# Kernel optimization log

Measured on AMD Instinct MI355X. Metric: run time of the kernel, lower is better.

## Reference

```python
import jax, jax.numpy as jnp
import numpy as np

B, I, H, N, E, SEQ = 16, 128, 32, 2048, 32768, 100


def setup_inputs() -> dict:
    key = jax.random.key(0)
    ks = jax.random.split(key, 8)
    s = lambda fan: 1.0 / np.sqrt(fan)
    return {
        "x": jax.random.normal(ks[0], (B, I), jnp.float32),
        "src": jax.random.randint(ks[1], (E,), 0, N, jnp.int32),
        "dst": jax.random.randint(ks[2], (E,), 0, N, jnp.int32),
        "Wr": jax.random.normal(ks[3], (I, H), jnp.float32) * s(I),
        "br": jnp.zeros((H,), jnp.float32),
        "Wz": jax.random.normal(ks[4], (I, H), jnp.float32) * s(I),
        "bz": jnp.zeros((H,), jnp.float32),
        "Wh": jax.random.normal(ks[5], (I, H), jnp.float32) * s(I),
        "bh": jnp.zeros((H,), jnp.float32),
        "Wg": jax.random.normal(ks[6], (H, H), jnp.float32) * s(H),
        "bg": jnp.zeros((H,), jnp.float32),
    }


def reference(x, src, dst, Wr, br, Wz, bz, Wh, bh, Wg, bg):
    # DGL GraphConv norm='both': edge weight 1/sqrt(deg_out[src]*deg_in[dst])
    ones = jnp.ones((E,), jnp.float32)
    deg_out = jnp.clip(jax.ops.segment_sum(ones, src, num_segments=N), 1.0)
    deg_in = jnp.clip(jax.ops.segment_sum(ones, dst, num_segments=N), 1.0)
    enorm = jax.lax.rsqrt(deg_out[src] * deg_in[dst])  # [E]

    # Input gates are constant over time (x is a single context vector)
    xr = (x @ Wr + br)[:, None, :]  # [B,1,H]
    xz = (x @ Wz + bz)[:, None, :]
    xh = (x @ Wh + bh)[:, None, :]

    def step(h, _):
        # message passing: gather src, normalize, scatter-add to dst
        m = h[:, src, :] * enorm[None, :, None]            # [B,E,H]
        agg = jnp.zeros_like(h).at[:, dst, :].add(m)       # [B,N,H]
        h_conv = agg @ Wg + bg                             # [B,N,H]
        r = jax.nn.sigmoid(xr + h_conv)
        z = jax.nn.sigmoid(xz + h_conv)
        h_tilde = jnp.tanh(xh + r * h_conv)
        h_new = (1.0 - z) * h + z * h_tilde
        return h_new, h_new

    h0 = jnp.zeros((B, N, H), jnp.float32)
    _, outs = jax.lax.scan(step, h0, None, length=SEQ)     # [SEQ,B,N,H]
    return jnp.transpose(outs, (1, 0, 2, 3)).reshape(B, -1)
```

## Files before the change

kernel.cpp:

```cpp
#include <hip/hip_runtime.h>
#include <math.h>

#define BATCH 16
#define IN 128
#define HD 32
#define NN 2048
#define NE 32768
#define SEQ 100
#define TPB 512
#define NBLK 512
#define GSZ 32
#define NGRP (NBLK / GSZ)
#define NXCD 8
#define MAXJ 64
#define ECAP 1536


__global__ void count_deg(const int* __restrict__ src, const int* __restrict__ dst,
                          int* deg_out, int* deg_in) {
    int e = blockIdx.x * blockDim.x + threadIdx.x;
    if (e < NE) {
        atomicAdd(&deg_out[src[e]], 1);
        atomicAdd(&deg_in[dst[e]], 1);
    }
}

__global__ void scan_rowptr(const int* __restrict__ deg_in, int* __restrict__ row_ptr) {
    __shared__ int partial[256];
    int t = threadIdx.x;
    int base = t * 8;
    int vals[8];
    int s = 0;
    for (int j = 0; j < 8; j++) { vals[j] = deg_in[base + j]; s += vals[j]; }
    partial[t] = s;
    __syncthreads();
    if (t == 0) {
        int acc = 0;
        for (int i = 0; i < 256; i++) { int v = partial[i]; partial[i] = acc; acc += v; }
        row_ptr[NN] = acc;
    }
    __syncthreads();
    int acc = partial[t];
    for (int j = 0; j < 8; j++) { row_ptr[base + j] = acc; acc += vals[j]; }
}

__global__ void scatter_edges(const int* __restrict__ src, const int* __restrict__ dst,
                              const int* __restrict__ deg_out, const int* __restrict__ deg_in,
                              const int* __restrict__ row_ptr, int* __restrict__ cursor,
                              int* __restrict__ col_idx, float* __restrict__ wgt) {
    int e = blockIdx.x * blockDim.x + threadIdx.x;
    if (e < NE) {
        int s = src[e], d = dst[e];
        int pos = row_ptr[d] + atomicAdd(&cursor[d], 1);
        col_idx[pos] = s * HD;
        float doo = (float)max(deg_out[s], 1);
        float dii = (float)max(deg_in[d], 1);
        wgt[pos] = rsqrtf(doo * dii);
    }
}

__global__ void xgates(const float* __restrict__ x,
                       const float* __restrict__ Wr, const float* __restrict__ br,
                       const float* __restrict__ Wz, const float* __restrict__ bz,
                       const float* __restrict__ Wh, const float* __restrict__ bh,
                       float* __restrict__ xr, float* __restrict__ xz, float* __restrict__ xh) {
    int t = blockIdx.x * blockDim.x + threadIdx.x;
    if (t < BATCH * HD) {
        int b = t / HD, hh = t % HD;
        float ar = br[hh], az = bz[hh], ah = bh[hh];
        const float* xb = x + b * IN;
        for (int i = 0; i < IN; i++) {
            float xv = xb[i];
            ar += xv * Wr[i * HD + hh];
            az += xv * Wz[i * HD + hh];
            ah += xv * Wh[i * HD + hh];
        }
        xr[t] = ar; xz[t] = az; xh[t] = ah;
    }
}


__device__ __forceinline__ void global_barrier(unsigned* __restrict__ lvl1,
                                               unsigned* __restrict__ root,
                                               unsigned step) {
    __syncthreads();
    if (threadIdx.x == 0) {
        const int gid = blockIdx.x / GSZ;
        __builtin_amdgcn_fence(__ATOMIC_RELEASE, "agent");
        __hip_atomic_fetch_add(&lvl1[gid * 32], 1u, __ATOMIC_RELAXED,
                               __HIP_MEMORY_SCOPE_AGENT);
        if ((blockIdx.x % GSZ) == 0) {
            while (__hip_atomic_load(&lvl1[gid * 32], __ATOMIC_RELAXED,
                                     __HIP_MEMORY_SCOPE_AGENT) < GSZ * step)
                __builtin_amdgcn_s_sleep(2);
            __hip_atomic_fetch_add(root, 1u, __ATOMIC_RELAXED,
                                   __HIP_MEMORY_SCOPE_AGENT);
        }
        while (__hip_atomic_load(root, __ATOMIC_RELAXED,
                                 __HIP_MEMORY_SCOPE_AGENT) < NGRP * step)
            __builtin_amdgcn_s_sleep(2);
        __builtin_amdgcn_fence(__ATOMIC_ACQUIRE, "agent");
    }
    __syncthreads();
}

__device__ __forceinline__ void xcd_barrier(unsigned* __restrict__ xcnt,
                                            unsigned* __restrict__ xgo,
                                            int xid, int slot, int cnt, unsigned s) {
    __syncthreads();
    if (threadIdx.x == 0) {
        __hip_atomic_fetch_add(&xcnt[xid * 32], 1u, __ATOMIC_RELAXED,
                               __HIP_MEMORY_SCOPE_AGENT);
        if (slot == 0) {
            while (__hip_atomic_load(&xcnt[xid * 32], __ATOMIC_RELAXED,
                                     __HIP_MEMORY_SCOPE_AGENT) < (unsigned)cnt * s)
                __builtin_amdgcn_s_sleep(1);
            __hip_atomic_store(&xgo[xid * 32], s, __ATOMIC_RELAXED,
                               __HIP_MEMORY_SCOPE_AGENT);
        } else {
            while (__hip_atomic_load(&xgo[xid * 32], __ATOMIC_RELAXED,
                                     __HIP_MEMORY_SCOPE_AGENT) < s)
                __builtin_amdgcn_s_sleep(1);
        }
    }
    __syncthreads();
    asm volatile("buffer_inv sc0\n\ts_waitcnt vmcnt(0)" ::: "memory");
}


__device__ __forceinline__ float fast_sigmoid(float x) {
    return __builtin_amdgcn_rcpf(1.f + __expf(-x));
}

__global__ void __launch_bounds__(TPB) gru_persistent(
    float* __restrict__ hA, float* __restrict__ hB,
    const int* __restrict__ row_ptr, const int* __restrict__ col_idx,
    const float* __restrict__ wgt,
    const float* __restrict__ Wg, const float* __restrict__ bg,
    const float* __restrict__ xr, const float* __restrict__ xz,
    const float* __restrict__ xh,
    float* __restrict__ out,
    unsigned* __restrict__ glvl1, unsigned* __restrict__ groot,
    unsigned* __restrict__ xreg, unsigned* __restrict__ xcnt,
    unsigned* __restrict__ xgo)
{
    __shared__ float aggL[TPB];
    __shared__ int jn[MAXJ], jrs[MAXJ], jraw[MAXJ], jplen[MAXJ], jofs[MAXJ];
    __shared__ __align__(16) int2 eLDS[ECAP];
    __shared__ int shr_slot, shr_cnt, shr_mode, shr_use;

    const int tid = threadIdx.x;
    const int lane = tid & 63;
    const int wid = tid >> 6;
    const int half = lane >> 5;
    const int l = lane & 31;

    int xraw;
    asm volatile("s_getreg_b32 %0, hwreg(HW_REG_XCC_ID)" : "=s"(xraw));
    int xid = xraw & 7;

    if (tid == 0)
        shr_slot = (int)__hip_atomic_fetch_add(&xreg[xid * 32], 1u, __ATOMIC_RELAXED,
                                               __HIP_MEMORY_SCOPE_AGENT);
    __syncthreads();
    int slot = shr_slot;

    global_barrier(glvl1, groot, 1u);

    if (tid == 0) {
        int sum = 0, mode = 1, mycnt = 0;
        for (int xx = 0; xx < NXCD; xx++) {
            int c = (int)__hip_atomic_load(&xreg[xx * 32], __ATOMIC_RELAXED,
                                           __HIP_MEMORY_SCOPE_AGENT);
            sum += c;
            if (c < 32) mode = 0;
            if (xx == xid) mycnt = c;
        }
        if (sum != NBLK) mode = 0;
        shr_mode = mode;
        shr_cnt = mycnt;
    }
    __syncthreads();
    const int xmode = shr_mode;
    int cnt = shr_cnt;
    if (!xmode) { xid = blockIdx.x & 7; slot = blockIdx.x >> 3; cnt = NBLK / NXCD; }
    const int wtot = cnt * 8;

    if (tid < MAXJ) {
        int k = tid >> 3, w = tid & 7;
        int n = slot * 8 + w + k * wtot;
        if (n < NN) {
            int rs = row_ptr[n], re = row_ptr[n + 1];
            jn[tid] = n; jrs[tid] = rs; jraw[tid] = re - rs;
            jplen[tid] = (re - rs + 7) & ~7;
        } else {
            jn[tid] = -1; jrs[tid] = 0; jraw[tid] = 0; jplen[tid] = 0;
        }
    }
    __syncthreads();
    if (tid == 0) {
        int o = 0;
        for (int j = 0; j < MAXJ; j++) { jofs[j] = o; o += jplen[j]; }
        shr_use = (o <= ECAP);
    }
    __syncthreads();
    const bool use_lds = (shr_use != 0);

    if (use_lds) {
        for (int k = 0; k < 8; k++) {
            int j = k * 8 + wid;
            if (jn[j] < 0) break;
            int rs = jrs[j], raw = jraw[j], pl = jplen[j], of = jofs[j];
            for (int i = lane; i < pl; i += 64) {
                int2 v;
                if (i < raw) { v.x = col_idx[rs + i] << 2; v.y = __float_as_int(wgt[rs + i]); }
                else         { v.x = 0; v.y = 0; }
                eLDS[of + i] = v;
            }
        }
    }
    __syncthreads();

    const int bb = 2 * xid + half;
    const float xrv = xr[bb * HD + l];
    const float xzv = xz[bb * HD + l];
    const float xhv = xh[bb * HD + l];
    const float bgv = bg[l];
    float wgreg[HD];
#pragma unroll
    for (int k = 0; k < HD; k++) wgreg[k] = Wg[k * HD + l];

    const int hoffb = (bb * (NN * HD) + l) * 4;
    float* outp = out + (size_t)bb * SEQ * (NN * HD) + l;

    const char* hprev = (const char*)hA;
    char* hnext = (char*)hB;

    for (int t = 0; t < SEQ; t++) {
        for (int k = 0; k < 8; k++) {
            const int j = k * 8 + wid;
            const int n = jn[j];
            if (n < 0) break;

            float agg = 0.f;
            if (use_lds) {
                const int4* ep = (const int4*)&eLDS[jofs[j]];
                const int pl = jplen[j];
                for (int e = 0; e < pl; e += 8) {
                    int4 p0 = ep[0], p1 = ep[1], p2 = ep[2], p3 = ep[3];
                    ep += 4;
                    float v0 = *(const float*)(hprev + (hoffb + p0.x));
                    float v1 = *(const float*)(hprev + (hoffb + p0.z));
                    float v2 = *(const float*)(hprev + (hoffb + p1.x));
                    float v3 = *(const float*)(hprev + (hoffb + p1.z));
                    float v4 = *(const float*)(hprev + (hoffb + p2.x));
                    float v5 = *(const float*)(hprev + (hoffb + p2.z));
                    float v6 = *(const float*)(hprev + (hoffb + p3.x));
                    float v7 = *(const float*)(hprev + (hoffb + p3.z));
                    agg = fmaf(__int_as_float(p0.y), v0, agg);
                    agg = fmaf(__int_as_float(p0.w), v1, agg);
                    agg = fmaf(__int_as_float(p1.y), v2, agg);
                    agg = fmaf(__int_as_float(p1.w), v3, agg);
                    agg = fmaf(__int_as_float(p2.y), v4, agg);
                    agg = fmaf(__int_as_float(p2.w), v5, agg);
                    agg = fmaf(__int_as_float(p3.y), v6, agg);
                    agg = fmaf(__int_as_float(p3.w), v7, agg);
                }
            } else {
                const int rs = jrs[j], re = rs + jraw[j];
                for (int e = rs; e < re; e++) {
                    int cb = col_idx[e] << 2;
                    agg = fmaf(wgt[e], *(const float*)(hprev + (hoffb + cb)), agg);
                }
            }

            aggL[tid] = agg;
            const float4* arow = (const float4*)&aggL[(tid & ~63) + (half << 5)];
            float conv = bgv;
#pragma unroll
            for (int kq = 0; kq < 8; kq++) {
                float4 a4 = arow[kq];
                conv = fmaf(a4.x, wgreg[4 * kq + 0], conv);
                conv = fmaf(a4.y, wgreg[4 * kq + 1], conv);
                conv = fmaf(a4.z, wgreg[4 * kq + 2], conv);
                conv = fmaf(a4.w, wgreg[4 * kq + 3], conv);
            }

            const float r = fast_sigmoid(xrv + conv);
            const float z = fast_sigmoid(xzv + conv);
            const float e2 = __expf(2.f * (xhv + r * conv));
            const float ht = 1.f - 2.f * __builtin_amdgcn_rcpf(e2 + 1.f);
            const int nb = hoffb + (n << 7);
            const float hp = *(const float*)(hprev + nb);
            const float hn = (1.f - z) * hp + z * ht;

            *(float*)(hnext + nb) = hn;
            __builtin_nontemporal_store(hn, outp + (n << 5));
        }
        if (t != SEQ - 1) {
            if (xmode)
                xcd_barrier(xcnt, xgo, xid, slot, cnt, (unsigned)(t + 1));
            else
                global_barrier(glvl1, groot, (unsigned)(t + 2));
        }
        char* tmp = (char*)hprev; hprev = hnext; hnext = tmp;
        outp += NN * HD;
    }
}


extern "C" void kernel_launch(void* const* d_in, const int* in_sizes, int n_in,
                              void* d_out, int out_size, void* d_ws, size_t ws_size,
                              hipStream_t stream) {
    const float* x   = (const float*)d_in[0];
    const int*   src = (const int*)d_in[1];
    const int*   dst = (const int*)d_in[2];
    const float* Wr  = (const float*)d_in[3];
    const float* br  = (const float*)d_in[4];
    const float* Wz  = (const float*)d_in[5];
    const float* bz  = (const float*)d_in[6];
    const float* Wh  = (const float*)d_in[7];
    const float* bh  = (const float*)d_in[8];
    const float* Wg  = (const float*)d_in[9];
    const float* bg  = (const float*)d_in[10];
    float* out = (float*)d_out;

    char* ws = (char*)d_ws;
    float* h0 = (float*)ws;            ws += (size_t)BATCH * NN * HD * 4;
    float* h1 = (float*)ws;            ws += (size_t)BATCH * NN * HD * 4;
    float* xr = (float*)ws;            ws += BATCH * HD * 4;
    float* xz = (float*)ws;            ws += BATCH * HD * 4;
    float* xh = (float*)ws;            ws += BATCH * HD * 4;
    int* deg_out = (int*)ws;           ws += NN * 4;
    int* deg_in  = (int*)ws;           ws += NN * 4;
    int* cursor  = (int*)ws;           ws += NN * 4;
    int* row_ptr = (int*)ws;           ws += (NN + 1) * 4;
    int* col_idx = (int*)ws;           ws += NE * 4;
    float* wgt   = (float*)ws;         ws += NE * 4;
    unsigned* glvl1 = (unsigned*)ws;   ws += NGRP * 32 * 4;
    unsigned* groot = (unsigned*)ws;   ws += 32 * 4;
    unsigned* xreg  = (unsigned*)ws;   ws += NXCD * 32 * 4;
    unsigned* xcnt  = (unsigned*)ws;   ws += NXCD * 32 * 4;
    unsigned* xgo   = (unsigned*)ws;   ws += NXCD * 32 * 4;

    hipMemsetAsync(h0, 0, (size_t)BATCH * NN * HD * 4, stream);
    hipMemsetAsync(deg_out, 0, 3 * NN * 4, stream);
    hipMemsetAsync(glvl1, 0, (NGRP * 32 + 32 + 3 * NXCD * 32) * 4, stream);

    count_deg<<<NE / 256, 256, 0, stream>>>(src, dst, deg_out, deg_in);
    scan_rowptr<<<1, 256, 0, stream>>>(deg_in, row_ptr);
    scatter_edges<<<NE / 256, 256, 0, stream>>>(src, dst, deg_out, deg_in, row_ptr,
                                                cursor, col_idx, wgt);
    xgates<<<2, 256, 0, stream>>>(x, Wr, br, Wz, bz, Wh, bh, xr, xz, xh);

    gru_persistent<<<dim3(NBLK), dim3(TPB), 0, stream>>>(
        h0, h1, row_ptr, col_idx, wgt, Wg, bg, xr, xz, xh, out,
        glvl1, groot, xreg, xcnt, xgo);
}
```

Before: 790.1 us.

## Shard XCD barrier counters, unroll edge gather by 16, fuse GRU update

The per-XCD barrier arrival counter is split into 8 padded sub-counters that the leader sums while polling, spreading atomic contention across cache lines. The LDS-edge aggregation loop is unrolled to 16 edges per iteration with an 8-edge tail, so more independent gather loads are in flight. The final GRU blend is rewritten as a single fma. The cost is a slightly slower leader poll (8 loads per check) and more register pressure from the wider unroll.

```diff
diff --git a/kernel.cpp b/kernel.cpp
--- a/kernel.cpp
+++ b/kernel.cpp
@@ -109,12 +109,18 @@
                                             int xid, int slot, int cnt, unsigned s) {
     __syncthreads();
     if (threadIdx.x == 0) {
-        __hip_atomic_fetch_add(&xcnt[xid * 32], 1u, __ATOMIC_RELAXED,
-                               __HIP_MEMORY_SCOPE_AGENT);
+        __hip_atomic_fetch_add(&xcnt[(xid * 8 + (slot & 7)) * 32], 1u,
+                               __ATOMIC_RELAXED, __HIP_MEMORY_SCOPE_AGENT);
         if (slot == 0) {
-            while (__hip_atomic_load(&xcnt[xid * 32], __ATOMIC_RELAXED,
-                                     __HIP_MEMORY_SCOPE_AGENT) < (unsigned)cnt * s)
+            for (;;) {
+                unsigned sum = 0;
+#pragma unroll
+                for (int i = 0; i < 8; i++)
+                    sum += __hip_atomic_load(&xcnt[(xid * 8 + i) * 32],
+                                             __ATOMIC_RELAXED, __HIP_MEMORY_SCOPE_AGENT);
+                if (sum >= (unsigned)cnt * s) break;
                 __builtin_amdgcn_s_sleep(1);
+            }
             __hip_atomic_store(&xgo[xid * 32], s, __ATOMIC_RELAXED,
                                __HIP_MEMORY_SCOPE_AGENT);
         } else {
@@ -246,9 +252,46 @@
             if (use_lds) {
                 const int4* ep = (const int4*)&eLDS[jofs[j]];
                 const int pl = jplen[j];
-                for (int e = 0; e < pl; e += 8) {
+                int e = 0;
+                for (; e + 16 <= pl; e += 16) {
                     int4 p0 = ep[0], p1 = ep[1], p2 = ep[2], p3 = ep[3];
-                    ep += 4;
+                    int4 p4 = ep[4], p5 = ep[5], p6 = ep[6], p7 = ep[7];
+                    ep += 8;
+                    float v0 = *(const float*)(hprev + (hoffb + p0.x));
+                    float v1 = *(const float*)(hprev + (hoffb + p0.z));
+                    float v2 = *(const float*)(hprev + (hoffb + p1.x));
+                    float v3 = *(const float*)(hprev + (hoffb + p1.z));
+                    float v4 = *(const float*)(hprev + (hoffb + p2.x));
+                    float v5 = *(const float*)(hprev + (hoffb + p2.z));
+                    float v6 = *(const float*)(hprev + (hoffb + p3.x));
+                    float v7 = *(const float*)(hprev + (hoffb + p3.z));
+                    float v8 = *(const float*)(hprev + (hoffb + p4.x));
+                    float v9 = *(const float*)(hprev + (hoffb + p4.z));
+                    float va = *(const float*)(hprev + (hoffb + p5.x));
+                    float vb = *(const float*)(hprev + (hoffb + p5.z));
+                    float vc = *(const float*)(hprev + (hoffb + p6.x));
+                    float vd = *(const float*)(hprev + (hoffb + p6.z));
+                    float ve = *(const float*)(hprev + (hoffb + p7.x));
+                    float vf = *(const float*)(hprev + (hoffb + p7.z));
+                    agg = fmaf(__int_as_float(p0.y), v0, agg);
+                    agg = fmaf(__int_as_float(p0.w), v1, agg);
+                    agg = fmaf(__int_as_float(p1.y), v2, agg);
+                    agg = fmaf(__int_as_float(p1.w), v3, agg);
+                    agg = fmaf(__int_as_float(p2.y), v4, agg);
+                    agg = fmaf(__int_as_float(p2.w), v5, agg);
+                    agg = fmaf(__int_as_float(p3.y), v6, agg);
+                    agg = fmaf(__int_as_float(p3.w), v7, agg);
+                    agg = fmaf(__int_as_float(p4.y), v8, agg);
+                    agg = fmaf(__int_as_float(p4.w), v9, agg);
+                    agg = fmaf(__int_as_float(p5.y), va, agg);
+                    agg = fmaf(__int_as_float(p5.w), vb, agg);
+                    agg = fmaf(__int_as_float(p6.y), vc, agg);
+                    agg = fmaf(__int_as_float(p6.w), vd, agg);
+                    agg = fmaf(__int_as_float(p7.y), ve, agg);
+                    agg = fmaf(__int_as_float(p7.w), vf, agg);
+                }
+                if (e < pl) {
+                    int4 p0 = ep[0], p1 = ep[1], p2 = ep[2], p3 = ep[3];
                     float v0 = *(const float*)(hprev + (hoffb + p0.x));
                     float v1 = *(const float*)(hprev + (hoffb + p0.z));
                     float v2 = *(const float*)(hprev + (hoffb + p1.x));
@@ -292,7 +335,7 @@
             const float ht = 1.f - 2.f * __builtin_amdgcn_rcpf(e2 + 1.f);
             const int nb = hoffb + (n << 7);
             const float hp = *(const float*)(hprev + nb);
-            const float hn = (1.f - z) * hp + z * ht;
+            const float hn = fmaf(z, ht - hp, hp);
 
             *(float*)(hnext + nb) = hn;
             __builtin_nontemporal_store(hn, outp + (n << 5));
@@ -340,12 +383,13 @@
     unsigned* glvl1 = (unsigned*)ws;   ws += NGRP * 32 * 4;
     unsigned* groot = (unsigned*)ws;   ws += 32 * 4;
     unsigned* xreg  = (unsigned*)ws;   ws += NXCD * 32 * 4;
-    unsigned* xcnt  = (unsigned*)ws;   ws += NXCD * 32 * 4;
+    unsigned* xcnt  = (unsigned*)ws;   ws += NXCD * 8 * 32 * 4;
     unsigned* xgo   = (unsigned*)ws;   ws += NXCD * 32 * 4;
 
     hipMemsetAsync(h0, 0, (size_t)BATCH * NN * HD * 4, stream);
     hipMemsetAsync(deg_out, 0, 3 * NN * 4, stream);
-    hipMemsetAsync(glvl1, 0, (NGRP * 32 + 32 + 3 * NXCD * 32) * 4, stream);
+    hipMemsetAsync(glvl1, 0,
+                   (NGRP * 32 + 32 + NXCD * 32 + NXCD * 8 * 32 + NXCD * 32) * 4, stream);
 
     count_deg<<<NE / 256, 256, 0, stream>>>(src, dst, deg_out, deg_in);
     scan_rowptr<<<1, 256, 0, stream>>>(deg_in, row_ptr);
```

Result: faster. 740.5 us (-6.3%).

## Process two hidden channels per lane and pair nodes per wavefront

Applied to the files above, without the earlier changes.

Each lane now handles two hidden channels with 8-byte vector gathers, and each wavefront processes two nodes at once (one per half-wave). This halves the inner-loop trip count and doubles bytes per load. Edge-list lengths are padded to the max of each paired node so the half-waves run the same trip count. The first timestep is computed analytically from a zero state, which removes the h0 memset and the first gather pass. The per-XCD barrier counter is split into 8 padded sub-counters to reduce atomic contention, and launch bounds now request 4 waves per SIMD, which trades register headroom for occupancy.

```diff
diff --git a/kernel.cpp b/kernel.cpp
--- a/kernel.cpp
+++ b/kernel.cpp
@@ -14,6 +14,9 @@
 #define NXCD 8
 #define MAXJ 64
 #define ECAP 1536
+
+using f32x2 = __attribute__((ext_vector_type(2))) float;
+using f32x4 = __attribute__((ext_vector_type(4))) float;
 
 
 __global__ void count_deg(const int* __restrict__ src, const int* __restrict__ dst,
@@ -109,12 +112,18 @@
                                             int xid, int slot, int cnt, unsigned s) {
     __syncthreads();
     if (threadIdx.x == 0) {
-        __hip_atomic_fetch_add(&xcnt[xid * 32], 1u, __ATOMIC_RELAXED,
-                               __HIP_MEMORY_SCOPE_AGENT);
+        __hip_atomic_fetch_add(&xcnt[(xid * 8 + (slot & 7)) * 32], 1u,
+                               __ATOMIC_RELAXED, __HIP_MEMORY_SCOPE_AGENT);
         if (slot == 0) {
-            while (__hip_atomic_load(&xcnt[xid * 32], __ATOMIC_RELAXED,
-                                     __HIP_MEMORY_SCOPE_AGENT) < (unsigned)cnt * s)
+            for (;;) {
+                unsigned sum = 0;
+#pragma unroll
+                for (int i = 0; i < 8; i++)
+                    sum += __hip_atomic_load(&xcnt[(xid * 8 + i) * 32],
+                                             __ATOMIC_RELAXED, __HIP_MEMORY_SCOPE_AGENT);
+                if (sum >= (unsigned)cnt * s) break;
                 __builtin_amdgcn_s_sleep(1);
+            }
             __hip_atomic_store(&xgo[xid * 32], s, __ATOMIC_RELAXED,
                                __HIP_MEMORY_SCOPE_AGENT);
         } else {
@@ -132,7 +141,27 @@
     return __builtin_amdgcn_rcpf(1.f + __expf(-x));
 }
 
-__global__ void __launch_bounds__(TPB) gru_persistent(
+__device__ __forceinline__ f32x2 gru_gate2(f32x2 conv, f32x2 xr2, f32x2 xz2,
+                                           f32x2 xh2, f32x2 hp) {
+    f32x2 hn;
+    {
+        float r = fast_sigmoid(xr2.x + conv.x);
+        float z = fast_sigmoid(xz2.x + conv.x);
+        float e2 = __expf(2.f * (xh2.x + r * conv.x));
+        float ht = 1.f - 2.f * __builtin_amdgcn_rcpf(e2 + 1.f);
+        hn.x = fmaf(z, ht - hp.x, hp.x);
+    }
+    {
+        float r = fast_sigmoid(xr2.y + conv.y);
+        float z = fast_sigmoid(xz2.y + conv.y);
+        float e2 = __expf(2.f * (xh2.y + r * conv.y));
+        float ht = 1.f - 2.f * __builtin_amdgcn_rcpf(e2 + 1.f);
+        hn.y = fmaf(z, ht - hp.y, hp.y);
+    }
+    return hn;
+}
+
+__global__ void __launch_bounds__(TPB, 4) gru_persistent(
     float* __restrict__ hA, float* __restrict__ hB,
     const int* __restrict__ row_ptr, const int* __restrict__ col_idx,
     const float* __restrict__ wgt,
@@ -144,7 +173,7 @@
     unsigned* __restrict__ xreg, unsigned* __restrict__ xcnt,
     unsigned* __restrict__ xgo)
 {
-    __shared__ float aggL[TPB];
+    __shared__ f32x2 aggL2[TPB];
     __shared__ int jn[MAXJ], jrs[MAXJ], jraw[MAXJ], jplen[MAXJ], jofs[MAXJ];
     __shared__ __align__(16) int2 eLDS[ECAP];
     __shared__ int shr_slot, shr_cnt, shr_mode, shr_use;
@@ -153,7 +182,8 @@
     const int lane = tid & 63;
     const int wid = tid >> 6;
     const int half = lane >> 5;
-    const int l = lane & 31;
+    const int bi = (lane >> 4) & 1;
+    const int cp = lane & 15;
 
     int xraw;
     asm volatile("s_getreg_b32 %0, hwreg(HW_REG_XCC_ID)" : "=s"(xraw));
@@ -197,6 +227,11 @@
             jn[tid] = -1; jrs[tid] = 0; jraw[tid] = 0; jplen[tid] = 0;
         }
     }
+    __syncthreads();
+    int pmax = 0;
+    if (tid < MAXJ) pmax = max(jplen[tid], jplen[tid ^ 8]);
+    __syncthreads();
+    if (tid < MAXJ && jn[tid] >= 0) jplen[tid] = pmax;
     __syncthreads();
     if (tid == 0) {
         int o = 0;
@@ -221,87 +256,107 @@
     }
     __syncthreads();
 
-    const int bb = 2 * xid + half;
-    const float xrv = xr[bb * HD + l];
-    const float xzv = xz[bb * HD + l];
-    const float xhv = xh[bb * HD + l];
-    const float bgv = bg[l];
-    float wgreg[HD];
+    const int bb = 2 * xid + bi;
+    const f32x2 xr2 = *(const f32x2*)&xr[bb * HD + 2 * cp];
+    const f32x2 xz2 = *(const f32x2*)&xz[bb * HD + 2 * cp];
+    const f32x2 xh2 = *(const f32x2*)&xh[bb * HD + 2 * cp];
+    const f32x2 bg2 = *(const f32x2*)&bg[2 * cp];
+    f32x2 wgreg2[HD];
 #pragma unroll
-    for (int k = 0; k < HD; k++) wgreg[k] = Wg[k * HD + l];
-
-    const int hoffb = (bb * (NN * HD) + l) * 4;
-    float* outp = out + (size_t)bb * SEQ * (NN * HD) + l;
+    for (int k = 0; k < HD; k++) wgreg2[k] = *(const f32x2*)&Wg[k * HD + 2 * cp];
+
+    const int hoffb = bb * (NN * HD) * 4 + cp * 8;
+    float* outp = out + (size_t)bb * SEQ * (NN * HD) + 2 * cp;
 
     const char* hprev = (const char*)hA;
     char* hnext = (char*)hB;
 
-    for (int t = 0; t < SEQ; t++) {
-        for (int k = 0; k < 8; k++) {
-            const int j = k * 8 + wid;
-            const int n = jn[j];
-            if (n < 0) break;
-
-            float agg = 0.f;
+    {
+        f32x2 zero2; zero2.x = 0.f; zero2.y = 0.f;
+        const f32x2 hn2 = gru_gate2(bg2, xr2, xz2, xh2, zero2);
+        for (int p = 0; p < 4; p++) {
+            const int n = jn[(2 * p + half) * 8 + wid];
+            if (n >= 0) {
+                *(f32x2*)(hnext + (hoffb + (n << 7))) = hn2;
+                __builtin_nontemporal_store(hn2, (f32x2*)(outp + n * HD));
+            }
+        }
+    }
+    if (xmode) xcd_barrier(xcnt, xgo, xid, slot, cnt, 1u);
+    else       global_barrier(glvl1, groot, 2u);
+    { char* tmp = (char*)hprev; hprev = hnext; hnext = tmp; }
+    outp += NN * HD;
+
+    for (int t = 1; t < SEQ; t++) {
+        for (int p = 0; p < 4; p++) {
+            const int jj = (2 * p + half) * 8 + wid;
+            const int n = jn[jj];
+            const int pl = jplen[jj];
+
+            f32x2 agg2; agg2.x = 0.f; agg2.y = 0.f;
             if (use_lds) {
-                const int4* ep = (const int4*)&eLDS[jofs[j]];
-                const int pl = jplen[j];
+                const int4* ep = (const int4*)&eLDS[jofs[jj]];
                 for (int e = 0; e < pl; e += 8) {
-                    int4 p0 = ep[0], p1 = ep[1], p2 = ep[2], p3 = ep[3];
+                    int4 q0 = ep[0], q1 = ep[1], q2 = ep[2], q3 = ep[3];
                     ep += 4;
-                    float v0 = *(const float*)(hprev + (hoffb + p0.x));
-                    float v1 = *(const float*)(hprev + (hoffb + p0.z));
-                    float v2 = *(const float*)(hprev + (hoffb + p1.x));
-                    float v3 = *(const float*)(hprev + (hoffb + p1.z));
-                    float v4 = *(const float*)(hprev + (hoffb + p2.x));
-                    float v5 = *(const float*)(hprev + (hoffb + p2.z));
-                    float v6 = *(const float*)(hprev + (hoffb + p3.x));
-                    float v7 = *(const float*)(hprev + (hoffb + p3.z));
-                    agg = fmaf(__int_as_float(p0.y), v0, agg);
-                    agg = fmaf(__int_as_float(p0.w), v1, agg);
-                    agg = fmaf(__int_as_float(p1.y), v2, agg);
-                    agg = fmaf(__int_as_float(p1.w), v3, agg);
-                    agg = fmaf(__int_as_float(p2.y), v4, agg);
-                    agg = fmaf(__int_as_float(p2.w), v5, agg);
-                    agg = fmaf(__int_as_float(p3.y), v6, agg);
-                    agg = fmaf(__int_as_float(p3.w), v7, agg);
+                    f32x2 v0 = *(const f32x2*)(hprev + (hoffb + q0.x));
+                    f32x2 v1 = *(const f32x2*)(hprev + (hoffb + q0.z));
+                    f32x2 v2 = *(const f32x2*)(hprev + (hoffb + q1.x));
+                    f32x2 v3 = *(const f32x2*)(hprev + (hoffb + q1.z));
+                    f32x2 v4 = *(const f32x2*)(hprev + (hoffb + q2.x));
+                    f32x2 v5 = *(const f32x2*)(hprev + (hoffb + q2.z));
+                    f32x2 v6 = *(const f32x2*)(hprev + (hoffb + q3.x));
+                    f32x2 v7 = *(const f32x2*)(hprev + (hoffb + q3.z));
+                    float w0 = __int_as_float(q0.y), w1 = __int_as_float(q0.w);
+                    float w2 = __int_as_float(q1.y), w3 = __int_as_float(q1.w);
+                    float w4 = __int_as_float(q2.y), w5 = __int_as_float(q2.w);
+                    float w6 = __int_as_float(q3.y), w7 = __int_as_float(q3.w);
+                    agg2.x = fmaf(w0, v0.x, agg2.x); agg2.y = fmaf(w0, v0.y, agg2.y);
+                    agg2.x = fmaf(w1, v1.x, agg2.x); agg2.y = fmaf(w1, v1.y, agg2.y);
+                    agg2.x = fmaf(w2, v2.x, agg2.x); agg2.y = fmaf(w2, v2.y, agg2.y);
+                    agg2.x = fmaf(w3, v3.x, agg2.x); agg2.y = fmaf(w3, v3.y, agg2.y);
+                    agg2.x = fmaf(w4, v4.x, agg2.x); agg2.y = fmaf(w4, v4.y, agg2.y);
+                    agg2.x = fmaf(w5, v5.x, agg2.x); agg2.y = fmaf(w5, v5.y, agg2.y);
+                    agg2.x = fmaf(w6, v6.x, agg2.x); agg2.y = fmaf(w6, v6.y, agg2.y);
+                    agg2.x = fmaf(w7, v7.x, agg2.x); agg2.y = fmaf(w7, v7.y, agg2.y);
                 }
             } else {
-                const int rs = jrs[j], re = rs + jraw[j];
+                const int rs = jrs[jj], re = rs + jraw[jj];
                 for (int e = rs; e < re; e++) {
                     int cb = col_idx[e] << 2;
-                    agg = fmaf(wgt[e], *(const float*)(hprev + (hoffb + cb)), agg);
+                    float w = wgt[e];
+                    f32x2 v = *(const f32x2*)(hprev + (hoffb + cb));
+                    agg2.x = fmaf(w, v.x, agg2.x);
+                    agg2.y = fmaf(w, v.y, agg2.y);
                 }
             }
 
-            aggL[tid] = agg;
-            const float4* arow = (const float4*)&aggL[(tid & ~63) + (half << 5)];
-            float conv = bgv;
+            aggL2[tid] = agg2;
+            const f32x4* arow = (const f32x4*)((const float*)aggL2 + (tid & ~15) * 2);
+            f32x2 conv2 = bg2;
 #pragma unroll
             for (int kq = 0; kq < 8; kq++) {
-                float4 a4 = arow[kq];
-                conv = fmaf(a4.x, wgreg[4 * kq + 0], conv);
-                conv = fmaf(a4.y, wgreg[4 * kq + 1], conv);
-                conv = fmaf(a4.z, wgreg[4 * kq + 2], conv);
-                conv = fmaf(a4.w, wgreg[4 * kq + 3], conv);
-            }
-
-            const float r = fast_sigmoid(xrv + conv);
-            const float z = fast_sigmoid(xzv + conv);
-            const float e2 = __expf(2.f * (xhv + r * conv));
-            const float ht = 1.f - 2.f * __builtin_amdgcn_rcpf(e2 + 1.f);
-            const int nb = hoffb + (n << 7);
-            const float hp = *(const float*)(hprev + nb);
-            const float hn = (1.f - z) * hp + z * ht;
-
-            *(float*)(hnext + nb) = hn;
-            __builtin_nontemporal_store(hn, outp + (n << 5));
-        }
+                f32x4 a4 = arow[kq];
+                f32x2 w0 = wgreg2[4 * kq + 0], w1 = wgreg2[4 * kq + 1];
+                f32x2 w2 = wgreg2[4 * kq + 2], w3 = wgreg2[4 * kq + 3];
+                conv2.x = fmaf(a4.x, w0.x, conv2.x); conv2.y = fmaf(a4.x, w0.y, conv2.y);
+                conv2.x = fmaf(a4.y, w1.x, conv2.x); conv2.y = fmaf(a4.y, w1.y, conv2.y);
+                conv2.x = fmaf(a4.z, w2.x, conv2.x); conv2.y = fmaf(a4.z, w2.y, conv2.y);
+                conv2.x = fmaf(a4.w, w3.x, conv2.x); conv2.y = fmaf(a4.w, w3.y, conv2.y);
+            }
+
+            if (n >= 0) {
+                const int nb = hoffb + (n << 7);
+                const f32x2 hp2 = *(const f32x2*)(hprev + nb);
+                const f32x2 hn2 = gru_gate2(conv2, xr2, xz2, xh2, hp2);
+                *(f32x2*)(hnext + nb) = hn2;
+                __builtin_nontemporal_store(hn2, (f32x2*)(outp + n * HD));
+            }
+        }
+
         if (t != SEQ - 1) {
-            if (xmode)
-                xcd_barrier(xcnt, xgo, xid, slot, cnt, (unsigned)(t + 1));
-            else
-                global_barrier(glvl1, groot, (unsigned)(t + 2));
+            if (xmode) xcd_barrier(xcnt, xgo, xid, slot, cnt, (unsigned)(t + 1));
+            else       global_barrier(glvl1, groot, (unsigned)(t + 2));
         }
         char* tmp = (char*)hprev; hprev = hnext; hnext = tmp;
         outp += NN * HD;
@@ -340,12 +395,12 @@
     unsigned* glvl1 = (unsigned*)ws;   ws += NGRP * 32 * 4;
     unsigned* groot = (unsigned*)ws;   ws += 32 * 4;
     unsigned* xreg  = (unsigned*)ws;   ws += NXCD * 32 * 4;
-    unsigned* xcnt  = (unsigned*)ws;   ws += NXCD * 32 * 4;
+    unsigned* xcnt  = (unsigned*)ws;   ws += NXCD * 8 * 32 * 4;
     unsigned* xgo   = (unsigned*)ws;   ws += NXCD * 32 * 4;
 
-    hipMemsetAsync(h0, 0, (size_t)BATCH * NN * HD * 4, stream);
     hipMemsetAsync(deg_out, 0, 3 * NN * 4, stream);
-    hipMemsetAsync(glvl1, 0, (NGRP * 32 + 32 + 3 * NXCD * 32) * 4, stream);
+    hipMemsetAsync(glvl1, 0,
+                   (NGRP * 32 + 32 + NXCD * 32 + NXCD * 8 * 32 + NXCD * 32) * 4, stream);
 
     count_deg<<<NE / 256, 256, 0, stream>>>(src, dst, deg_out, deg_in);
     scan_rowptr<<<1, 256, 0, stream>>>(deg_in, row_ptr);
```

Result: slower. 881.1 us (+11.5%).
